# Optimization experiments

Measured on AMD Instinct MI355X. Metric: run time of the kernel, lower is better.

## Reference

```python
import jax, jax.numpy as jnp
import numpy as np

B = 32           # graphs in batch
N_PER = 512      # nodes per graph
N = B * N_PER    # 16384 total nodes (block-diagonal batched graph)
E = N * 16       # 262144 edges
D_IN = 128
D_OUT = 128
ASSIGN = 2048    # total clusters = B * K
K = ASSIGN // B  # 64 clusters per graph


def setup_inputs() -> dict:
    key = jax.random.key(0)
    ks = jax.random.split(key, 6)
    h = jax.random.normal(ks[0], (N, D_IN), jnp.float32)
    # edges confined within each graph -> block-diagonal batched adjacency
    gid = jnp.repeat(jnp.arange(B), E // B)
    edge_src = (jax.random.randint(ks[1], (E,), 0, N_PER) + gid * N_PER).astype(jnp.int32)
    edge_dst = (jax.random.randint(ks[2], (E,), 0, N_PER) + gid * N_PER).astype(jnp.int32)
    # GraphSage NodeApply linears: Linear(2*in, out)
    stdv_f = 1.0 / np.sqrt(2 * D_IN)
    W_feat = jax.random.uniform(ks[3], (2 * D_IN, D_OUT), jnp.float32, -stdv_f, stdv_f)
    b_feat = jnp.zeros((D_OUT,), jnp.float32)
    W_pool = jax.random.uniform(ks[4], (2 * D_IN, ASSIGN), jnp.float32, -stdv_f, stdv_f)
    b_pool = jnp.zeros((ASSIGN,), jnp.float32)
    return {"h": h, "W_feat": W_feat, "b_feat": b_feat,
            "W_pool": W_pool, "b_pool": b_pool,
            "edge_src": edge_src, "edge_dst": edge_dst}


def _graphsage(h, W, b, src, dst):
    # mean aggregation over in-neighbors (dropout=0, batch_norm off)
    msg = jax.ops.segment_sum(h[src], dst, num_segments=N)          # [N, d_in]
    deg = jax.ops.segment_sum(jnp.ones((src.shape[0],), h.dtype), dst, num_segments=N)
    h_neigh = msg / jnp.maximum(deg, 1.0)[:, None]
    bundle = jnp.concatenate([h, h_neigh], axis=1) @ W + b          # [N, d_out]
    # F.normalize(p=2, dim=1) then activation, as in GraphSage NodeApply
    norm = jnp.linalg.norm(bundle, axis=1, keepdims=True)
    bundle = bundle / jnp.maximum(norm, 1e-12)
    return jax.nn.relu(bundle)


def _forward(h, W_feat, b_feat, W_pool, b_pool, src, dst):
    feat = _graphsage(h, W_feat, b_feat, src, dst)       # [N, D_OUT]
    assign = _graphsage(h, W_pool, b_pool, src, dst)     # [N, ASSIGN]
    # block-diagonal mask: node i of graph g may only assign to g's K clusters
    gid_n = jnp.arange(N) // N_PER                       # [N]
    gid_c = jnp.arange(ASSIGN) // K                      # [ASSIGN]
    mask = (gid_n[:, None] == gid_c[None, :]).astype(jnp.float32)
    # masked_softmax with memory_efficient=False
    s = jax.nn.softmax(assign * mask, axis=-1) * mask
    s = s / (s.sum(axis=-1, keepdims=True) + 1e-13)      # [N, ASSIGN]
    h_new = s.T @ feat                                   # [ASSIGN, D_OUT]
    # adj_new = S^T A S without densifying A: (A S)[dst] += S[src]
    a_s = jax.ops.segment_sum(s[src], dst, num_segments=N)
    adj_new = s.T @ a_s                                  # [ASSIGN, ASSIGN]
    return adj_new, h_new


def reference(h, W_feat, b_feat, W_pool, b_pool, edge_src, edge_dst):
    return _forward(h, W_feat, b_feat, W_pool, b_pool, edge_src, edge_dst)
```

## Files before the change

### kernel.cpp

```cpp
#include <hip/hip_runtime.h>

#define NB   32
#define NPER 512
#define NN   16384
#define EE   262144
#define DD   128
#define AS   2048
#define KC   64

using short8   = __attribute__((ext_vector_type(8))) short;
using floatx4  = __attribute__((ext_vector_type(4))) float;
using ushort4v = __attribute__((ext_vector_type(4))) unsigned short;

typedef __attribute__((address_space(3))) unsigned int lds_u32;
typedef const __attribute__((address_space(1))) unsigned int gbl_u32;

static __device__ __forceinline__ void gload16(const unsigned short* g, unsigned short* l) {
    __builtin_amdgcn_global_load_lds((gbl_u32*)g, (lds_u32*)l, 16, 0, 0);
}

static __device__ __forceinline__ float bits2f(unsigned int u) {
    union { unsigned int i; float f; } z; z.i = u << 16; return z.f;
}
static __device__ __forceinline__ unsigned short f2b(float x) {
    union { float f; unsigned int u; } v; v.f = x;
    unsigned int r = v.u + 0x7fffu + ((v.u >> 16) & 1u);
    return (unsigned short)(r >> 16);
}

__global__ void prep_kernel(const float* __restrict__ h, unsigned short* __restrict__ bundle,
                            unsigned short* __restrict__ hT, const int* __restrict__ esrc,
                            const int* __restrict__ edst, unsigned int* __restrict__ Acnt) {
    __shared__ unsigned short fT[128 * 136];
    int b = blockIdx.x, t = threadIdx.x;
    if (b < 128) {
        int node0 = b * 128;
        int r = t >> 1, hf = t & 1;
        const float4* h4 = reinterpret_cast<const float4*>(h + (size_t)(node0 + r) * 128 + hf * 64);
        unsigned short* bo = bundle + (size_t)(node0 + r) * 256 + hf * 64;
#pragma unroll
        for (int i = 0; i < 16; i++) {
            float4 v = h4[i];
            ushort4v o = { f2b(v.x), f2b(v.y), f2b(v.z), f2b(v.w) };
            *reinterpret_cast<ushort4v*>(bo + 4 * i) = o;
            int c = hf * 64 + 4 * i;
            fT[(c + 0) * 136 + r] = o.x;
            fT[(c + 1) * 136 + r] = o.y;
            fT[(c + 2) * 136 + r] = o.z;
            fT[(c + 3) * 136 + r] = o.w;
        }
        __syncthreads();
        int c = t >> 1, nh = t & 1;
        const uint4* src = reinterpret_cast<const uint4*>(&fT[c * 136 + nh * 64]);
        uint4* dst = reinterpret_cast<uint4*>(hT + (size_t)c * NN + node0 + nh * 64);
#pragma unroll
        for (int i = 0; i < 8; i++) dst[i] = src[i];
    } else {
        int e = (b - 128) * 256 + t;
        int d = edst[e], sl = esrc[e] & 511;
        int idx = d * 512 + sl;
        atomicAdd(&Acnt[idx >> 2], 1u << (8 * (idx & 3)));
    }
}

__global__ void conv_kernel(const unsigned int* __restrict__ Acnt,
                            unsigned short* __restrict__ Aadj, float* __restrict__ invdeg) {
    int t = threadIdx.x;
    int row = blockIdx.x * 8 + (t >> 5);
    int u = t & 31;
    uint4 w = reinterpret_cast<const uint4*>(Acnt)[(size_t)row * 32 + u];
    unsigned int wa[4] = { w.x, w.y, w.z, w.w };
    unsigned short out[16];
    float sum = 0.f;
#pragma unroll
    for (int i = 0; i < 4; i++) {
#pragma unroll
        for (int bb = 0; bb < 4; bb++) {
            float fv = (float)((wa[i] >> (8 * bb)) & 0xffu);
            sum += fv;
            out[4 * i + bb] = f2b(fv);
        }
    }
    unsigned int pw[8];
#pragma unroll
    for (int i = 0; i < 8; i++)
        pw[i] = (unsigned int)out[2 * i] | ((unsigned int)out[2 * i + 1] << 16);
    uint4* dst = reinterpret_cast<uint4*>(Aadj + (size_t)row * 512 + u * 16);
    uint4 s0 = { pw[0], pw[1], pw[2], pw[3] }, s1 = { pw[4], pw[5], pw[6], pw[7] };
    dst[0] = s0; dst[1] = s1;
#pragma unroll
    for (int d = 1; d < 32; d <<= 1) sum += __shfl_xor(sum, d, 64);
    if (u == 0) invdeg[row] = 1.0f / fmaxf(sum, 1.0f);
}

__global__ void transpose_cast2_kernel(const float* __restrict__ Wf, const float* __restrict__ Wp,
                                       unsigned short* __restrict__ WfT, unsigned short* __restrict__ WpT) {
    __shared__ float tl[32][33];
    int tx = threadIdx.x, ty = threadIdx.y;
    int bx = blockIdx.x;
    const float* in; unsigned short* out; int C, cb;
    if (bx < DD / 32) { in = Wf; out = WfT; C = DD; cb = bx; }
    else              { in = Wp; out = WpT; C = AS; cb = bx - DD / 32; }
    int c0 = cb * 32, r0 = blockIdx.y * 32;
    for (int i = 0; i < 4; i++)
        tl[ty + 8 * i][tx] = in[(size_t)(r0 + ty + 8 * i) * C + c0 + tx];
    __syncthreads();
    for (int i = 0; i < 4; i++)
        out[(size_t)(c0 + ty + 8 * i) * 256 + r0 + tx] = f2b(tl[tx][ty + 8 * i]);
}

__global__ __launch_bounds__(256) void agg_h_mfma_kernel(
    const unsigned short* __restrict__ Aadj, const unsigned short* __restrict__ hT,
    const float* __restrict__ invdeg, unsigned short* __restrict__ bundle) {
    __shared__ alignas(16) unsigned short lA[64 * 512];
    int tid = threadIdx.x, bx = blockIdx.x;
    int r0 = bx * 64, g = bx >> 3;
    int wv = tid >> 6, lane = tid & 63, q = lane >> 4, lm = lane & 15;
    int mw = wv >> 1, nw = wv & 1;
#pragma unroll
    for (int j = 0; j < 16; j++) {
        int u = tid + 256 * j;
        int row = u >> 6, cu = (u & 63) ^ (row & 7);
        gload16(Aadj + (size_t)(r0 + row) * 512 + cu * 8, &lA[u * 8]);
    }
    floatx4 acc[2][4];
#pragma unroll
    for (int mt = 0; mt < 2; mt++)
#pragma unroll
        for (int nt = 0; nt < 4; nt++) acc[mt][nt] = (floatx4)0.f;
    __syncthreads();

    const unsigned short* Bb = hT + (size_t)(64 * nw + lm) * NN + g * 512 + (q << 3);
    short8 bF[2][4];
#pragma unroll
    for (int nt = 0; nt < 4; nt++)
        bF[0][nt] = *reinterpret_cast<const short8*>(Bb + (size_t)16 * nt * NN);
    for (int ki = 0; ki < 16; ki++) {
        if (ki < 15) {
#pragma unroll
            for (int nt = 0; nt < 4; nt++)
                bF[(ki + 1) & 1][nt] =
                    *reinterpret_cast<const short8*>(Bb + (size_t)16 * nt * NN + (ki + 1) * 32);
        }
        short8 aF[2];
        int swz = (4 * ki + q) ^ (lm & 7);
#pragma unroll
        for (int mt = 0; mt < 2; mt++)
            aF[mt] = *reinterpret_cast<const short8*>(&lA[((32 * mw + 16 * mt + lm) * 64 + swz) * 8]);
#pragma unroll
        for (int mt = 0; mt < 2; mt++)
#pragma unroll
            for (int nt = 0; nt < 4; nt++)
                acc[mt][nt] = __builtin_amdgcn_mfma_f32_16x16x32_bf16(aF[mt], bF[ki & 1][nt],
                                                                      acc[mt][nt], 0, 0, 0);
    }
#pragma unroll
    for (int mt = 0; mt < 2; mt++)
#pragma unroll
        for (int r = 0; r < 4; r++) {
            int row = 32 * mw + 16 * mt + 4 * q + r;
            float inv = invdeg[r0 + row];
#pragma unroll
            for (int nt = 0; nt < 4; nt++)
                bundle[(size_t)(r0 + row) * 256 + 128 + 64 * nw + 16 * nt + lm] =
                    f2b(acc[mt][nt][r] * inv);
        }
}

__global__ __launch_bounds__(256) void feat_mfma_kernel(
    const unsigned short* __restrict__ bundle, const unsigned short* __restrict__ WfT,
    const float* __restrict__ bfe, unsigned short* __restrict__ featT) {
    __shared__ alignas(16) unsigned short lA[512 * 8];
    __shared__ alignas(16) unsigned short lB[512 * 8];
    __shared__ float red[256];
    __shared__ alignas(16) unsigned short fT[128 * 136];
    int tid = threadIdx.x;
    int r0 = blockIdx.x * 128;
    int wv = tid >> 6, lane = tid & 63;
    int mw = wv >> 1, nw = wv & 1, q = lane >> 4, lm = lane & 15;
    int rowS0 = tid >> 2,         cS0 = (tid & 3) ^ ((rowS0 >> 1) & 3);
    int rowS1 = (tid + 256) >> 2, cS1 = ((tid + 256) & 3) ^ ((rowS1 >> 1) & 3);
    int swz = q ^ ((lm >> 1) & 3);

    floatx4 acc[4][4];
#pragma unroll
    for (int mi = 0; mi < 4; mi++)
#pragma unroll
        for (int ni = 0; ni < 4; ni++) acc[mi][ni] = (floatx4)0.f;

    for (int k0 = 0; k0 < 256; k0 += 32) {
        gload16(bundle + (size_t)(r0 + rowS0) * 256 + k0 + 8 * cS0, &lA[tid * 8]);
        gload16(bundle + (size_t)(r0 + rowS1) * 256 + k0 + 8 * cS1, &lA[(tid + 256) * 8]);
        gload16(WfT + (size_t)rowS0 * 256 + k0 + 8 * cS0, &lB[tid * 8]);
        gload16(WfT + (size_t)rowS1 * 256 + k0 + 8 * cS1, &lB[(tid + 256) * 8]);
        __syncthreads();
        short8 aF[4], bF[4];
#pragma unroll
        for (int mi = 0; mi < 4; mi++)
            aF[mi] = *reinterpret_cast<const short8*>(&lA[((64 * mw + 16 * mi + lm) * 4 + swz) * 8]);
#pragma unroll
        for (int ni = 0; ni < 4; ni++)
            bF[ni] = *reinterpret_cast<const short8*>(&lB[((64 * nw + 16 * ni + lm) * 4 + swz) * 8]);
#pragma unroll
        for (int mi = 0; mi < 4; mi++)
#pragma unroll
            for (int ni = 0; ni < 4; ni++)
                acc[mi][ni] = __builtin_amdgcn_mfma_f32_16x16x32_bf16(aF[mi], bF[ni], acc[mi][ni], 0, 0, 0);
        __syncthreads();
    }
#pragma unroll
    for (int ni = 0; ni < 4; ni++) {
        float bv = bfe[64 * nw + 16 * ni + lm];
#pragma unroll
        for (int mi = 0; mi < 4; mi++)
#pragma unroll
            for (int r = 0; r < 4; r++) acc[mi][ni][r] += bv;
    }
#pragma unroll
    for (int mi = 0; mi < 4; mi++)
#pragma unroll
        for (int r = 0; r < 4; r++) {
            float p = 0.f;
#pragma unroll
            for (int ni = 0; ni < 4; ni++) p += acc[mi][ni][r] * acc[mi][ni][r];
            p += __shfl_xor(p, 1, 64);
            p += __shfl_xor(p, 2, 64);
            p += __shfl_xor(p, 4, 64);
            p += __shfl_xor(p, 8, 64);
            if (lm == 0) red[nw * 128 + 64 * mw + 16 * mi + 4 * q + r] = p;
        }
    __syncthreads();
#pragma unroll
    for (int mi = 0; mi < 4; mi++) {
        float rrn[4];
#pragma unroll
        for (int r = 0; r < 4; r++) {
            int rl = 64 * mw + 16 * mi + 4 * q + r;
            rrn[r] = 1.0f / fmaxf(sqrtf(red[rl] + red[128 + rl]), 1e-12f);
        }
#pragma unroll
        for (int ni = 0; ni < 4; ni++) {
            int col = 64 * nw + 16 * ni + lm;
            ushort4v pk = { f2b(fmaxf(acc[mi][ni][0] * rrn[0], 0.f)),
                            f2b(fmaxf(acc[mi][ni][1] * rrn[1], 0.f)),
                            f2b(fmaxf(acc[mi][ni][2] * rrn[2], 0.f)),
                            f2b(fmaxf(acc[mi][ni][3] * rrn[3], 0.f)) };
            *reinterpret_cast<ushort4v*>(&fT[col * 136 + 64 * mw + 16 * mi + 4 * q]) = pk;
        }
    }
    __syncthreads();
    {
        int col = tid >> 1, half = tid & 1;
        const uint4* src = reinterpret_cast<const uint4*>(&fT[col * 136 + half * 64]);
        uint4* dst = reinterpret_cast<uint4*>(featT + (size_t)col * NN + r0 + half * 64);
#pragma unroll
        for (int i = 0; i < 8; i++) dst[i] = src[i];
    }
}

__global__ __launch_bounds__(256) void pool_fused_kernel(
    const unsigned short* __restrict__ bundle, const unsigned short* __restrict__ WpT,
    const float* __restrict__ bp, unsigned short* __restrict__ sT) {
    __shared__ alignas(16) unsigned short lA[2048 * 8];
    __shared__ float raw[64 * 68];
    __shared__ float ssq_l[4 * 64];
    __shared__ float rn_l[64];
    int tid = threadIdx.x, bx = blockIdx.x;
    int r0 = bx * 64, g = bx >> 3;
    int wv = tid >> 6, lane = tid & 63, q = lane >> 4, lm = lane & 15;

#pragma unroll
    for (int j = 0; j < 8; j++) {
        int u = tid + 256 * j;
        int row = u >> 5;
        int chunk = (u & 31) ^ (row & 7);
        gload16(bundle + (size_t)(r0 + row) * 256 + chunk * 8, &lA[u * 8]);
    }
    float ssqacc[4][4];
#pragma unroll
    for (int mi = 0; mi < 4; mi++)
#pragma unroll
        for (int r = 0; r < 4; r++) ssqacc[mi][r] = 0.f;
    __syncthreads();

    for (int nc8 = 0; nc8 < 8; nc8++) {
        int nc = 4 * nc8 + wv;
        const unsigned short* Bb = WpT + ((size_t)(nc * 64 + lm) << 8) + (q << 3);
        short8 bF[2][4];
#pragma unroll
        for (int ni = 0; ni < 4; ni++)
            bF[0][ni] = *reinterpret_cast<const short8*>(Bb + (ni << 12));
        floatx4 acc[4][4];
#pragma unroll
        for (int mi = 0; mi < 4; mi++)
#pragma unroll
            for (int ni = 0; ni < 4; ni++) acc[mi][ni] = (floatx4)0.f;
#pragma unroll
        for (int k = 0; k < 8; k++) {
            if (k < 7) {
#pragma unroll
                for (int ni = 0; ni < 4; ni++)
                    bF[(k + 1) & 1][ni] =
                        *reinterpret_cast<const short8*>(Bb + (ni << 12) + ((k + 1) << 5));
            }
            short8 aF[4];
            int swz = (4 * k + q) ^ (lm & 7);
#pragma unroll
            for (int mi = 0; mi < 4; mi++)
                aF[mi] = *reinterpret_cast<const short8*>(&lA[((16 * mi + lm) * 32 + swz) * 8]);
#pragma unroll
            for (int mi = 0; mi < 4; mi++)
#pragma unroll
                for (int ni = 0; ni < 4; ni++)
                    acc[mi][ni] = __builtin_amdgcn_mfma_f32_16x16x32_bf16(aF[mi], bF[k & 1][ni],
                                                                          acc[mi][ni], 0, 0, 0);
        }
        float bv[4];
#pragma unroll
        for (int ni = 0; ni < 4; ni++) bv[ni] = bp[nc * 64 + 16 * ni + lm];
#pragma unroll
        for (int mi = 0; mi < 4; mi++)
#pragma unroll
            for (int r = 0; r < 4; r++) {
                float p = 0.f;
#pragma unroll
                for (int ni = 0; ni < 4; ni++) {
                    acc[mi][ni][r] += bv[ni];
                    p += acc[mi][ni][r] * acc[mi][ni][r];
                }
                ssqacc[mi][r] += p;
            }
        if (nc == g) {
#pragma unroll
            for (int mi = 0; mi < 4; mi++)
#pragma unroll
                for (int ni = 0; ni < 4; ni++)
#pragma unroll
                    for (int r = 0; r < 4; r++)
                        raw[(16 * mi + 4 * q + r) * 68 + 16 * ni + lm] = acc[mi][ni][r];
        }
    }
#pragma unroll
    for (int mi = 0; mi < 4; mi++)
#pragma unroll
        for (int r = 0; r < 4; r++) {
            float p = ssqacc[mi][r];
            p += __shfl_xor(p, 1, 64);
            p += __shfl_xor(p, 2, 64);
            p += __shfl_xor(p, 4, 64);
            p += __shfl_xor(p, 8, 64);
            if (lm == 0) ssq_l[wv * 64 + 16 * mi + 4 * q + r] = p;
        }
    __syncthreads();
    if (tid < 64)
        rn_l[tid] = 1.0f / fmaxf(sqrtf(ssq_l[tid] + ssq_l[64 + tid] + ssq_l[128 + tid] +
                                       ssq_l[192 + tid]), 1e-12f);
    __syncthreads();
    {
        int row = tid >> 2, j = tid & 3;
        int nloc = ((bx & 7) << 6) + row;
        float rn = rn_l[row];
        float v[16];
        float mx = -1e30f;
#pragma unroll
        for (int c4 = 0; c4 < 4; c4++) {
            float4 rv = *reinterpret_cast<const float4*>(&raw[row * 68 + 16 * j + 4 * c4]);
            v[4 * c4 + 0] = fmaxf(rv.x * rn, 0.f);
            v[4 * c4 + 1] = fmaxf(rv.y * rn, 0.f);
            v[4 * c4 + 2] = fmaxf(rv.z * rn, 0.f);
            v[4 * c4 + 3] = fmaxf(rv.w * rn, 0.f);
        }
#pragma unroll
        for (int c = 0; c < 16; c++) mx = fmaxf(mx, v[c]);
        mx = fmaxf(mx, __shfl_xor(mx, 1, 64));
        mx = fmaxf(mx, __shfl_xor(mx, 2, 64));
        float z = 0.f;
#pragma unroll
        for (int c = 0; c < 16; c++) { v[c] = __expf(v[c] - mx); z += v[c]; }
        z += __shfl_xor(z, 1, 64);
        z += __shfl_xor(z, 2, 64);
        float iz = 1.0f / z;
#pragma unroll
        for (int c4 = 0; c4 < 4; c4++) {
            size_t tb = (size_t)(g * KC + 16 * j + 4 * c4) * NPER + nloc;
            sT[tb] = f2b(v[4 * c4 + 0] * iz);
            sT[tb + NPER] = f2b(v[4 * c4 + 1] * iz);
            sT[tb + 2 * NPER] = f2b(v[4 * c4 + 2] * iz);
            sT[tb + 3 * NPER] = f2b(v[4 * c4 + 3] * iz);
        }
    }
}

__global__ __launch_bounds__(256) void as_mfma_kernel(
    const unsigned short* __restrict__ sT, const unsigned short* __restrict__ Aadj,
    unsigned short* __restrict__ asT) {
    __shared__ alignas(16) unsigned short lS[64 * 512];
    int tid = threadIdx.x, bx = blockIdx.x;
    int g = bx >> 1, half = bx & 1;
    int wv = tid >> 6, lane = tid & 63, q = lane >> 4, lm = lane & 15;
#pragma unroll
    for (int j = 0; j < 16; j++) {
        int u = tid + 256 * j;
        int row = u >> 6, cu = (u & 63) ^ (row & 7);
        gload16(sT + (size_t)(g * KC + row) * NPER + cu * 8, &lS[u * 8]);
    }
    floatx4 acc[4][4];
#pragma unroll
    for (int mi = 0; mi < 4; mi++)
#pragma unroll
        for (int nt = 0; nt < 4; nt++) acc[mi][nt] = (floatx4)0.f;
    __syncthreads();

    int dbase = half * 256 + wv * 64;
    const unsigned short* Bb = Aadj + (size_t)(g * 512 + dbase + lm) * 512 + (q << 3);
    short8 bF[2][4];
#pragma unroll
    for (int nt = 0; nt < 4; nt++)
        bF[0][nt] = *reinterpret_cast<const short8*>(Bb + (size_t)16 * nt * 512);
    for (int ki = 0; ki < 16; ki++) {
        if (ki < 15) {
#pragma unroll
            for (int nt = 0; nt < 4; nt++)
                bF[(ki + 1) & 1][nt] =
                    *reinterpret_cast<const short8*>(Bb + (size_t)16 * nt * 512 + (ki + 1) * 32);
        }
        short8 aF[4];
        int swz = (4 * ki + q) ^ (lm & 7);
#pragma unroll
        for (int mi = 0; mi < 4; mi++)
            aF[mi] = *reinterpret_cast<const short8*>(&lS[((16 * mi + lm) * 64 + swz) * 8]);
#pragma unroll
        for (int mi = 0; mi < 4; mi++)
#pragma unroll
            for (int nt = 0; nt < 4; nt++)
                acc[mi][nt] = __builtin_amdgcn_mfma_f32_16x16x32_bf16(aF[mi], bF[ki & 1][nt],
                                                                      acc[mi][nt], 0, 0, 0);
    }
#pragma unroll
    for (int mi = 0; mi < 4; mi++)
#pragma unroll
        for (int r = 0; r < 4; r++) {
            int row = 16 * mi + 4 * q + r;
#pragma unroll
            for (int nt = 0; nt < 4; nt++)
                asT[(size_t)(g * KC + row) * NPER + dbase + 16 * nt + lm] = f2b(acc[mi][nt][r]);
        }
}

__global__ __launch_bounds__(256) void hnew_adj_kernel(
    const unsigned short* __restrict__ sT, const unsigned short* __restrict__ featT,
    const unsigned short* __restrict__ asT, float* __restrict__ adjf,
    float* __restrict__ hnewf) {
    __shared__ alignas(16) unsigned short lS[1024 * 8];
    __shared__ alignas(16) unsigned short lF[2048 * 8];
    __shared__ alignas(16) unsigned short lAS[1024 * 8];
    int tid = threadIdx.x;
    int ch = blockIdx.x, g = blockIdx.y;
    int k0 = g * NPER + ch * 128;
    int wv = tid >> 6, lane = tid & 63, q = lane >> 4, lm = lane & 15;

#pragma unroll
    for (int j = 0; j < 4; j++) {
        int u = tid + 256 * j;
        int row = u >> 4, cu = (u & 15) ^ (row & 15);
        gload16(sT + (size_t)(g * KC + row) * NPER + ch * 128 + cu * 8, &lS[u * 8]);
    }
#pragma unroll
    for (int j = 0; j < 8; j++) {
        int u = tid + 256 * j;
        int row = u >> 4, cu = (u & 15) ^ (row & 15);
        gload16(featT + (size_t)row * NN + k0 + cu * 8, &lF[u * 8]);
    }
#pragma unroll
    for (int j = 0; j < 4; j++) {
        int u = tid + 256 * j;
        int row = u >> 4, cu = (u & 15) ^ (row & 15);
        gload16(asT + (size_t)(g * KC + row) * NPER + ch * 128 + cu * 8, &lAS[u * 8]);
    }
    floatx4 acc[4][4];
#pragma unroll
    for (int mi = 0; mi < 4; mi++)
#pragma unroll
        for (int ni = 0; ni < 4; ni++) acc[mi][ni] = (floatx4)0.f;
    __syncthreads();

    bool isH = (wv < 2);
    for (int ks = 0; ks < 4; ks++) {
        if (!isH && (ks >> 1) != (wv & 1)) continue;
        short8 aF[4], bF[4];
#pragma unroll
        for (int mi = 0; mi < 4; mi++)
            aF[mi] = *reinterpret_cast<const short8*>(
                &lS[((16 * mi + lm) * 16 + ((4 * ks + q) ^ lm)) * 8]);
        if (isH) {
#pragma unroll
            for (int ni = 0; ni < 4; ni++)
                bF[ni] = *reinterpret_cast<const short8*>(
                    &lF[((64 * wv + 16 * ni + lm) * 16 + ((4 * ks + q) ^ lm)) * 8]);
        } else {
#pragma unroll
            for (int ni = 0; ni < 4; ni++)
                bF[ni] = *reinterpret_cast<const short8*>(
                    &lAS[((16 * ni + lm) * 16 + ((4 * ks + q) ^ lm)) * 8]);
        }
#pragma unroll
        for (int mi = 0; mi < 4; mi++)
#pragma unroll
            for (int ni = 0; ni < 4; ni++)
                acc[mi][ni] = __builtin_amdgcn_mfma_f32_16x16x32_bf16(aF[mi], bF[ni], acc[mi][ni], 0, 0, 0);
    }
    if (isH) {
#pragma unroll
        for (int mi = 0; mi < 4; mi++)
#pragma unroll
            for (int ni = 0; ni < 4; ni++)
#pragma unroll
                for (int r = 0; r < 4; r++)
                    atomicAdd(&hnewf[(size_t)(g * KC + 16 * mi + 4 * q + r) * DD +
                                     64 * wv + 16 * ni + lm], acc[mi][ni][r]);
    } else {
#pragma unroll
        for (int mi = 0; mi < 4; mi++)
#pragma unroll
            for (int ni = 0; ni < 4; ni++)
#pragma unroll
                for (int r = 0; r < 4; r++)
                    atomicAdd(&adjf[(size_t)(g * KC + 16 * mi + 4 * q + r) * AS +
                                    g * KC + 16 * ni + lm], acc[mi][ni][r]);
    }
}

extern "C" void kernel_launch(void* const* d_in, const int* in_sizes, int n_in,
                              void* d_out, int out_size, void* d_ws, size_t ws_size,
                              hipStream_t stream) {
    const float* h   = (const float*)d_in[0];
    const float* Wf  = (const float*)d_in[1];
    const float* bfe = (const float*)d_in[2];
    const float* Wp  = (const float*)d_in[3];
    const float* bp  = (const float*)d_in[4];
    const int* esrc  = (const int*)d_in[5];
    const int* edst  = (const int*)d_in[6];

    float* adjf  = (float*)d_out;
    float* hnewf = adjf + (size_t)AS * AS;

    unsigned short* bundle = (unsigned short*)d_ws;
    unsigned short* WfT   = bundle + (size_t)NN * 256;
    unsigned short* WpT   = WfT + 128 * 256;
    unsigned short* sT    = WpT + (size_t)AS * 256;
    unsigned short* asT   = sT + (size_t)NN * KC;
    unsigned short* featT = asT + (size_t)NN * KC;
    unsigned short* hT    = featT + (size_t)DD * NN;
    unsigned short* Aadj  = hT + (size_t)DD * NN;
    float* invdeg = (float*)(Aadj + (size_t)NN * 512);
    unsigned int* Acnt = (unsigned int*)(invdeg + NN);

    hipMemsetAsync(Acnt, 0, (size_t)NN * 512, stream);
    hipMemsetAsync(d_out, 0, ((size_t)AS * AS + (size_t)AS * DD) * sizeof(float), stream);

    prep_kernel<<<128 + EE / 256, 256, 0, stream>>>(h, bundle, hT, esrc, edst, Acnt);
    conv_kernel<<<NN / 8, 256, 0, stream>>>(Acnt, Aadj, invdeg);
    transpose_cast2_kernel<<<dim3(DD / 32 + AS / 32, 256 / 32), dim3(32, 8), 0, stream>>>(
        Wf, Wp, WfT, WpT);
    agg_h_mfma_kernel<<<NN / 64, 256, 0, stream>>>(Aadj, hT, invdeg, bundle);
    feat_mfma_kernel<<<NN / 128, 256, 0, stream>>>(bundle, WfT, bfe, featT);
    pool_fused_kernel<<<NN / 64, 256, 0, stream>>>(bundle, WpT, bp, sT);
    as_mfma_kernel<<<NB * 2, 256, 0, stream>>>(sT, Aadj, asT);
    hnew_adj_kernel<<<dim3(4, NB), 256, 0, stream>>>(sT, featT, asT, adjf, hnewf);
}
```

Baseline: 185.7 us.

## Fuse all stages into one cooperative persistent kernel with grid syncs

Replaces the two memsets and eight separate kernel launches with a single cooperative mega-kernel of 256 persistent blocks. Each stage runs as a grid-strided tile loop, stages are separated by grid.sync(), and a union sizes shared memory for the largest stage. This removes per-launch overhead and inter-kernel gaps. The cost is one-block-per-CU occupancy (launch_bounds 256,1, with LDS sized to the largest stage), stages with fewer tiles than blocks leaving CUs idle, and grid barrier cost. The old multi-kernel path stays as a fallback if the cooperative launch fails.

Measured after the change: 519.1 us. 180% more time.

```diff
diff --git a/kernel.cpp b/kernel.cpp
--- a/kernel.cpp
+++ b/kernel.cpp
@@ -1,4 +1,7 @@
 #include <hip/hip_runtime.h>
+#include <hip/hip_cooperative_groups.h>
+
+namespace cg = cooperative_groups;
 
 #define NB   32
 #define NPER 512
@@ -7,6 +10,7 @@
 #define DD   128
 #define AS   2048
 #define KC   64
+#define GRID 256
 
 using short8   = __attribute__((ext_vector_type(8))) short;
 using floatx4  = __attribute__((ext_vector_type(4))) float;
@@ -27,6 +31,518 @@
     unsigned int r = v.u + 0x7fffu + ((v.u >> 16) & 1u);
     return (unsigned short)(r >> 16);
 }
+
+union __align__(16) SMem {
+    unsigned short big[32768];
+    struct { unsigned short lA[16384]; float raw[4352]; float ssq[256]; float rn[64]; } pool;
+    struct { unsigned short lA[4096]; unsigned short lB[4096]; float red[256];
+             unsigned short fT[17408]; } feat;
+    struct { unsigned short lS[8192]; unsigned short lF[16384]; unsigned short lAS[8192]; } ha;
+    struct { unsigned short fT[17408]; } prep;
+    struct { float tl[32][33]; } tr;
+};
+
+__global__ __launch_bounds__(256, 1) void mega_kernel(
+    const float* __restrict__ h, const float* __restrict__ Wf, const float* __restrict__ bfe,
+    const float* __restrict__ Wp, const float* __restrict__ bp,
+    const int* __restrict__ esrc, const int* __restrict__ edst,
+    float* __restrict__ adjf, float* __restrict__ hnewf,
+    unsigned short* __restrict__ bundle, unsigned short* __restrict__ WfT,
+    unsigned short* __restrict__ WpT, unsigned short* __restrict__ sT,
+    unsigned short* __restrict__ asT, unsigned short* __restrict__ featT,
+    unsigned short* __restrict__ hT, unsigned short* __restrict__ Aadj,
+    float* __restrict__ invdeg, unsigned int* __restrict__ Acnt) {
+    __shared__ SMem sm;
+    cg::grid_group grid = cg::this_grid();
+    int tid = threadIdx.x;
+    int gtid = blockIdx.x * 256 + tid;
+
+    {
+        uint4 z = {0u, 0u, 0u, 0u};
+        uint4* A4 = reinterpret_cast<uint4*>(Acnt);
+        for (int i = gtid; i < 524288; i += GRID * 256) A4[i] = z;
+        uint4* O4 = reinterpret_cast<uint4*>(adjf);
+        for (int i = gtid; i < 1114112; i += GRID * 256) O4[i] = z;
+    }
+    __threadfence();
+    grid.sync();
+
+    for (int t = blockIdx.x; t < 1696; t += GRID) {
+        if (t < 128) {
+            int node0 = t * 128;
+            int r = tid >> 1, hf = tid & 1;
+            const float4* h4 = reinterpret_cast<const float4*>(h + (size_t)(node0 + r) * 128 + hf * 64);
+            unsigned short* bo = bundle + (size_t)(node0 + r) * 256 + hf * 64;
+#pragma unroll
+            for (int i = 0; i < 16; i++) {
+                float4 v = h4[i];
+                ushort4v o = { f2b(v.x), f2b(v.y), f2b(v.z), f2b(v.w) };
+                *reinterpret_cast<ushort4v*>(bo + 4 * i) = o;
+                int c = hf * 64 + 4 * i;
+                sm.prep.fT[(c + 0) * 136 + r] = o.x;
+                sm.prep.fT[(c + 1) * 136 + r] = o.y;
+                sm.prep.fT[(c + 2) * 136 + r] = o.z;
+                sm.prep.fT[(c + 3) * 136 + r] = o.w;
+            }
+            __syncthreads();
+            int c = tid >> 1, nh = tid & 1;
+            const uint4* src = reinterpret_cast<const uint4*>(&sm.prep.fT[c * 136 + nh * 64]);
+            uint4* dst = reinterpret_cast<uint4*>(hT + (size_t)c * NN + node0 + nh * 64);
+#pragma unroll
+            for (int i = 0; i < 8; i++) dst[i] = src[i];
+        } else if (t < 1152) {
+            int e = (t - 128) * 256 + tid;
+            int d = edst[e], sl = esrc[e] & 511;
+            int idx = d * 512 + sl;
+            atomicAdd(&Acnt[idx >> 2], 1u << (8 * (idx & 3)));
+        } else {
+            int tb = t - 1152;
+            int bx = tb % 68, by = tb / 68;
+            int tx = tid & 31, ty = tid >> 5;
+            const float* in; unsigned short* out; int C, cb;
+            if (bx < DD / 32) { in = Wf; out = WfT; C = DD; cb = bx; }
+            else              { in = Wp; out = WpT; C = AS; cb = bx - DD / 32; }
+            int c0 = cb * 32, r0 = by * 32;
+            for (int i = 0; i < 4; i++)
+                sm.tr.tl[ty + 8 * i][tx] = in[(size_t)(r0 + ty + 8 * i) * C + c0 + tx];
+            __syncthreads();
+            for (int i = 0; i < 4; i++)
+                out[(size_t)(c0 + ty + 8 * i) * 256 + r0 + tx] = f2b(sm.tr.tl[tx][ty + 8 * i]);
+        }
+        __syncthreads();
+    }
+    __threadfence();
+    grid.sync();
+
+    for (int t = blockIdx.x; t < 2048; t += GRID) {
+        int row = t * 8 + (tid >> 5);
+        int u = tid & 31;
+        uint4 w = reinterpret_cast<const uint4*>(Acnt)[(size_t)row * 32 + u];
+        unsigned int wa[4] = { w.x, w.y, w.z, w.w };
+        unsigned short out[16];
+        float sum = 0.f;
+#pragma unroll
+        for (int i = 0; i < 4; i++) {
+#pragma unroll
+            for (int bb = 0; bb < 4; bb++) {
+                float fv = (float)((wa[i] >> (8 * bb)) & 0xffu);
+                sum += fv;
+                out[4 * i + bb] = f2b(fv);
+            }
+        }
+        unsigned int pw[8];
+#pragma unroll
+        for (int i = 0; i < 8; i++)
+            pw[i] = (unsigned int)out[2 * i] | ((unsigned int)out[2 * i + 1] << 16);
+        uint4* dst = reinterpret_cast<uint4*>(Aadj + (size_t)row * 512 + u * 16);
+        uint4 s0 = { pw[0], pw[1], pw[2], pw[3] }, s1 = { pw[4], pw[5], pw[6], pw[7] };
+        dst[0] = s0; dst[1] = s1;
+#pragma unroll
+        for (int d = 1; d < 32; d <<= 1) sum += __shfl_xor(sum, d, 64);
+        if (u == 0) invdeg[row] = 1.0f / fmaxf(sum, 1.0f);
+    }
+    __threadfence();
+    grid.sync();
+
+    for (int bx = blockIdx.x; bx < 256; bx += GRID) {
+        int r0 = bx * 64, g = bx >> 3;
+        int wv = tid >> 6, lane = tid & 63, q = lane >> 4, lm = lane & 15;
+        int mw = wv >> 1, nw = wv & 1;
+#pragma unroll
+        for (int j = 0; j < 16; j++) {
+            int u = tid + 256 * j;
+            int row = u >> 6, cu = (u & 63) ^ (row & 7);
+            gload16(Aadj + (size_t)(r0 + row) * 512 + cu * 8, &sm.big[u * 8]);
+        }
+        floatx4 acc[2][4];
+#pragma unroll
+        for (int mt = 0; mt < 2; mt++)
+#pragma unroll
+            for (int nt = 0; nt < 4; nt++) acc[mt][nt] = (floatx4)0.f;
+        __syncthreads();
+
+        const unsigned short* Bb = hT + (size_t)(64 * nw + lm) * NN + g * 512 + (q << 3);
+        short8 bF[2][4];
+#pragma unroll
+        for (int nt = 0; nt < 4; nt++)
+            bF[0][nt] = *reinterpret_cast<const short8*>(Bb + (size_t)16 * nt * NN);
+        for (int ki = 0; ki < 16; ki++) {
+            if (ki < 15) {
+#pragma unroll
+                for (int nt = 0; nt < 4; nt++)
+                    bF[(ki + 1) & 1][nt] =
+                        *reinterpret_cast<const short8*>(Bb + (size_t)16 * nt * NN + (ki + 1) * 32);
+            }
+            short8 aF[2];
+            int swz = (4 * ki + q) ^ (lm & 7);
+#pragma unroll
+            for (int mt = 0; mt < 2; mt++)
+                aF[mt] = *reinterpret_cast<const short8*>(&sm.big[((32 * mw + 16 * mt + lm) * 64 + swz) * 8]);
+#pragma unroll
+            for (int mt = 0; mt < 2; mt++)
+#pragma unroll
+                for (int nt = 0; nt < 4; nt++)
+                    acc[mt][nt] = __builtin_amdgcn_mfma_f32_16x16x32_bf16(aF[mt], bF[ki & 1][nt],
+                                                                          acc[mt][nt], 0, 0, 0);
+        }
+#pragma unroll
+        for (int mt = 0; mt < 2; mt++)
+#pragma unroll
+            for (int r = 0; r < 4; r++) {
+                int row = 32 * mw + 16 * mt + 4 * q + r;
+                float inv = invdeg[r0 + row];
+#pragma unroll
+                for (int nt = 0; nt < 4; nt++)
+                    bundle[(size_t)(r0 + row) * 256 + 128 + 64 * nw + 16 * nt + lm] =
+                        f2b(acc[mt][nt][r] * inv);
+            }
+        __syncthreads();
+    }
+    __threadfence();
+    grid.sync();
+
+    for (int t = blockIdx.x; t < 384; t += GRID) {
+        if (t < 128) {
+            int r0 = t * 128;
+            int wv = tid >> 6, lane = tid & 63;
+            int mw = wv >> 1, nw = wv & 1, q = lane >> 4, lm = lane & 15;
+            int rowS0 = tid >> 2,         cS0 = (tid & 3) ^ ((rowS0 >> 1) & 3);
+            int rowS1 = (tid + 256) >> 2, cS1 = ((tid + 256) & 3) ^ ((rowS1 >> 1) & 3);
+            int swz = q ^ ((lm >> 1) & 3);
+            floatx4 acc[4][4];
+#pragma unroll
+            for (int mi = 0; mi < 4; mi++)
+#pragma unroll
+                for (int ni = 0; ni < 4; ni++) acc[mi][ni] = (floatx4)0.f;
+            for (int k0 = 0; k0 < 256; k0 += 32) {
+                gload16(bundle + (size_t)(r0 + rowS0) * 256 + k0 + 8 * cS0, &sm.feat.lA[tid * 8]);
+                gload16(bundle + (size_t)(r0 + rowS1) * 256 + k0 + 8 * cS1, &sm.feat.lA[(tid + 256) * 8]);
+                gload16(WfT + (size_t)rowS0 * 256 + k0 + 8 * cS0, &sm.feat.lB[tid * 8]);
+                gload16(WfT + (size_t)rowS1 * 256 + k0 + 8 * cS1, &sm.feat.lB[(tid + 256) * 8]);
+                __syncthreads();
+                short8 aF[4], bF[4];
+#pragma unroll
+                for (int mi = 0; mi < 4; mi++)
+                    aF[mi] = *reinterpret_cast<const short8*>(&sm.feat.lA[((64 * mw + 16 * mi + lm) * 4 + swz) * 8]);
+#pragma unroll
+                for (int ni = 0; ni < 4; ni++)
+                    bF[ni] = *reinterpret_cast<const short8*>(&sm.feat.lB[((64 * nw + 16 * ni + lm) * 4 + swz) * 8]);
+#pragma unroll
+                for (int mi = 0; mi < 4; mi++)
+#pragma unroll
+                    for (int ni = 0; ni < 4; ni++)
+                        acc[mi][ni] = __builtin_amdgcn_mfma_f32_16x16x32_bf16(aF[mi], bF[ni], acc[mi][ni], 0, 0, 0);
+                __syncthreads();
+            }
+#pragma unroll
+            for (int ni = 0; ni < 4; ni++) {
+                float bv = bfe[64 * nw + 16 * ni + lm];
+#pragma unroll
+                for (int mi = 0; mi < 4; mi++)
+#pragma unroll
+                    for (int r = 0; r < 4; r++) acc[mi][ni][r] += bv;
+            }
+#pragma unroll
+            for (int mi = 0; mi < 4; mi++)
+#pragma unroll
+                for (int r = 0; r < 4; r++) {
+                    float p = 0.f;
+#pragma unroll
+                    for (int ni = 0; ni < 4; ni++) p += acc[mi][ni][r] * acc[mi][ni][r];
+                    p += __shfl_xor(p, 1, 64);
+                    p += __shfl_xor(p, 2, 64);
+                    p += __shfl_xor(p, 4, 64);
+                    p += __shfl_xor(p, 8, 64);
+                    if (lm == 0) sm.feat.red[nw * 128 + 64 * mw + 16 * mi + 4 * q + r] = p;
+                }
+            __syncthreads();
+#pragma unroll
+            for (int mi = 0; mi < 4; mi++) {
+                float rrn[4];
+#pragma unroll
+                for (int r = 0; r < 4; r++) {
+                    int rl = 64 * mw + 16 * mi + 4 * q + r;
+                    rrn[r] = 1.0f / fmaxf(sqrtf(sm.feat.red[rl] + sm.feat.red[128 + rl]), 1e-12f);
+                }
+#pragma unroll
+                for (int ni = 0; ni < 4; ni++) {
+                    int col = 64 * nw + 16 * ni + lm;
+                    ushort4v pk = { f2b(fmaxf(acc[mi][ni][0] * rrn[0], 0.f)),
+                                    f2b(fmaxf(acc[mi][ni][1] * rrn[1], 0.f)),
+                                    f2b(fmaxf(acc[mi][ni][2] * rrn[2], 0.f)),
+                                    f2b(fmaxf(acc[mi][ni][3] * rrn[3], 0.f)) };
+                    *reinterpret_cast<ushort4v*>(&sm.feat.fT[col * 136 + 64 * mw + 16 * mi + 4 * q]) = pk;
+                }
+            }
+            __syncthreads();
+            {
+                int col = tid >> 1, half = tid & 1;
+                const uint4* src = reinterpret_cast<const uint4*>(&sm.feat.fT[col * 136 + half * 64]);
+                uint4* dst = reinterpret_cast<uint4*>(featT + (size_t)col * NN + r0 + half * 64);
+#pragma unroll
+                for (int i = 0; i < 8; i++) dst[i] = src[i];
+            }
+        } else {
+            int bx = t - 128;
+            int r0 = bx * 64, g = bx >> 3;
+            int wv = tid >> 6, lane = tid & 63, q = lane >> 4, lm = lane & 15;
+#pragma unroll
+            for (int j = 0; j < 8; j++) {
+                int u = tid + 256 * j;
+                int row = u >> 5;
+                int chunk = (u & 31) ^ (row & 7);
+                gload16(bundle + (size_t)(r0 + row) * 256 + chunk * 8, &sm.pool.lA[u * 8]);
+            }
+            float ssqacc[4][4];
+#pragma unroll
+            for (int mi = 0; mi < 4; mi++)
+#pragma unroll
+                for (int r = 0; r < 4; r++) ssqacc[mi][r] = 0.f;
+            __syncthreads();
+            for (int nc8 = 0; nc8 < 8; nc8++) {
+                int nc = 4 * nc8 + wv;
+                const unsigned short* Bb = WpT + ((size_t)(nc * 64 + lm) << 8) + (q << 3);
+                short8 bF[2][4];
+#pragma unroll
+                for (int ni = 0; ni < 4; ni++)
+                    bF[0][ni] = *reinterpret_cast<const short8*>(Bb + (ni << 12));
+                floatx4 acc[4][4];
+#pragma unroll
+                for (int mi = 0; mi < 4; mi++)
+#pragma unroll
+                    for (int ni = 0; ni < 4; ni++) acc[mi][ni] = (floatx4)0.f;
+#pragma unroll
+                for (int k = 0; k < 8; k++) {
+                    if (k < 7) {
+#pragma unroll
+                        for (int ni = 0; ni < 4; ni++)
+                            bF[(k + 1) & 1][ni] =
+                                *reinterpret_cast<const short8*>(Bb + (ni << 12) + ((k + 1) << 5));
+                    }
+                    short8 aF[4];
+                    int swz = (4 * k + q) ^ (lm & 7);
+#pragma unroll
+                    for (int mi = 0; mi < 4; mi++)
+                        aF[mi] = *reinterpret_cast<const short8*>(&sm.pool.lA[((16 * mi + lm) * 32 + swz) * 8]);
+#pragma unroll
+                    for (int mi = 0; mi < 4; mi++)
+#pragma unroll
+                        for (int ni = 0; ni < 4; ni++)
+                            acc[mi][ni] = __builtin_amdgcn_mfma_f32_16x16x32_bf16(aF[mi], bF[k & 1][ni],
+                                                                                  acc[mi][ni], 0, 0, 0);
+                }
+                float bv[4];
+#pragma unroll
+                for (int ni = 0; ni < 4; ni++) bv[ni] = bp[nc * 64 + 16 * ni + lm];
+#pragma unroll
+                for (int mi = 0; mi < 4; mi++)
+#pragma unroll
+                    for (int r = 0; r < 4; r++) {
+                        float p = 0.f;
+#pragma unroll
+                        for (int ni = 0; ni < 4; ni++) {
+                            acc[mi][ni][r] += bv[ni];
+                            p += acc[mi][ni][r] * acc[mi][ni][r];
+                        }
+                        ssqacc[mi][r] += p;
+                    }
+                if (nc == g) {
+#pragma unroll
+                    for (int mi = 0; mi < 4; mi++)
+#pragma unroll
+                        for (int ni = 0; ni < 4; ni++)
+#pragma unroll
+                            for (int r = 0; r < 4; r++)
+                                sm.pool.raw[(16 * mi + 4 * q + r) * 68 + 16 * ni + lm] = acc[mi][ni][r];
+                }
+            }
+#pragma unroll
+            for (int mi = 0; mi < 4; mi++)
+#pragma unroll
+                for (int r = 0; r < 4; r++) {
+                    float p = ssqacc[mi][r];
+                    p += __shfl_xor(p, 1, 64);
+                    p += __shfl_xor(p, 2, 64);
+                    p += __shfl_xor(p, 4, 64);
+                    p += __shfl_xor(p, 8, 64);
+                    if (lm == 0) sm.pool.ssq[wv * 64 + 16 * mi + 4 * q + r] = p;
+                }
+            __syncthreads();
+            if (tid < 64)
+                sm.pool.rn[tid] = 1.0f / fmaxf(sqrtf(sm.pool.ssq[tid] + sm.pool.ssq[64 + tid] +
+                                               sm.pool.ssq[128 + tid] + sm.pool.ssq[192 + tid]), 1e-12f);
+            __syncthreads();
+            {
+                int row = tid >> 2, j = tid & 3;
+                int nloc = ((bx & 7) << 6) + row;
+                float rn = sm.pool.rn[row];
+                float v[16];
+                float mx = -1e30f;
+#pragma unroll
+                for (int c4 = 0; c4 < 4; c4++) {
+                    float4 rv = *reinterpret_cast<const float4*>(&sm.pool.raw[row * 68 + 16 * j + 4 * c4]);
+                    v[4 * c4 + 0] = fmaxf(rv.x * rn, 0.f);
+                    v[4 * c4 + 1] = fmaxf(rv.y * rn, 0.f);
+                    v[4 * c4 + 2] = fmaxf(rv.z * rn, 0.f);
+                    v[4 * c4 + 3] = fmaxf(rv.w * rn, 0.f);
+                }
+#pragma unroll
+                for (int c = 0; c < 16; c++) mx = fmaxf(mx, v[c]);
+                mx = fmaxf(mx, __shfl_xor(mx, 1, 64));
+                mx = fmaxf(mx, __shfl_xor(mx, 2, 64));
+                float z = 0.f;
+#pragma unroll
+                for (int c = 0; c < 16; c++) { v[c] = __expf(v[c] - mx); z += v[c]; }
+                z += __shfl_xor(z, 1, 64);
+                z += __shfl_xor(z, 2, 64);
+                float iz = 1.0f / z;
+#pragma unroll
+                for (int c4 = 0; c4 < 4; c4++) {
+                    size_t tb = (size_t)(g * KC + 16 * j + 4 * c4) * NPER + nloc;
+                    sT[tb] = f2b(v[4 * c4 + 0] * iz);
+                    sT[tb + NPER] = f2b(v[4 * c4 + 1] * iz);
+                    sT[tb + 2 * NPER] = f2b(v[4 * c4 + 2] * iz);
+                    sT[tb + 3 * NPER] = f2b(v[4 * c4 + 3] * iz);
+                }
+            }
+        }
+        __syncthreads();
+    }
+    __threadfence();
+    grid.sync();
+
+    for (int bx = blockIdx.x; bx < NB * 2; bx += GRID) {
+        int g = bx >> 1, half = bx & 1;
+        int wv = tid >> 6, lane = tid & 63, q = lane >> 4, lm = lane & 15;
+#pragma unroll
+        for (int j = 0; j < 16; j++) {
+            int u = tid + 256 * j;
+            int row = u >> 6, cu = (u & 63) ^ (row & 7);
+            gload16(sT + (size_t)(g * KC + row) * NPER + cu * 8, &sm.big[u * 8]);
+        }
+        floatx4 acc[4][4];
+#pragma unroll
+        for (int mi = 0; mi < 4; mi++)
+#pragma unroll
+            for (int nt = 0; nt < 4; nt++) acc[mi][nt] = (floatx4)0.f;
+        __syncthreads();
+
+        int dbase = half * 256 + wv * 64;
+        const unsigned short* Bb = Aadj + (size_t)(g * 512 + dbase + lm) * 512 + (q << 3);
+        short8 bF[2][4];
+#pragma unroll
+        for (int nt = 0; nt < 4; nt++)
+            bF[0][nt] = *reinterpret_cast<const short8*>(Bb + (size_t)16 * nt * 512);
+        for (int ki = 0; ki < 16; ki++) {
+            if (ki < 15) {
+#pragma unroll
+                for (int nt = 0; nt < 4; nt++)
+                    bF[(ki + 1) & 1][nt] =
+                        *reinterpret_cast<const short8*>(Bb + (size_t)16 * nt * 512 + (ki + 1) * 32);
+            }
+            short8 aF[4];
+            int swz = (4 * ki + q) ^ (lm & 7);
+#pragma unroll
+            for (int mi = 0; mi < 4; mi++)
+                aF[mi] = *reinterpret_cast<const short8*>(&sm.big[((16 * mi + lm) * 64 + swz) * 8]);
+#pragma unroll
+            for (int mi = 0; mi < 4; mi++)
+#pragma unroll
+                for (int nt = 0; nt < 4; nt++)
+                    acc[mi][nt] = __builtin_amdgcn_mfma_f32_16x16x32_bf16(aF[mi], bF[ki & 1][nt],
+                                                                          acc[mi][nt], 0, 0, 0);
+        }
+#pragma unroll
+        for (int mi = 0; mi < 4; mi++)
+#pragma unroll
+            for (int r = 0; r < 4; r++) {
+                int row = 16 * mi + 4 * q + r;
+#pragma unroll
+                for (int nt = 0; nt < 4; nt++)
+                    asT[(size_t)(g * KC + row) * NPER + dbase + 16 * nt + lm] = f2b(acc[mi][nt][r]);
+            }
+        __syncthreads();
+    }
+    __threadfence();
+    grid.sync();
+
+    for (int t = blockIdx.x; t < 128; t += GRID) {
+        int ch = t & 3, g = t >> 2;
+        int k0 = g * NPER + ch * 128;
+        int wv = tid >> 6, lane = tid & 63, q = lane >> 4, lm = lane & 15;
+#pragma unroll
+        for (int j = 0; j < 4; j++) {
+            int u = tid + 256 * j;
+            int row = u >> 4, cu = (u & 15) ^ (row & 15);
+            gload16(sT + (size_t)(g * KC + row) * NPER + ch * 128 + cu * 8, &sm.ha.lS[u * 8]);
+        }
+#pragma unroll
+        for (int j = 0; j < 8; j++) {
+            int u = tid + 256 * j;
+            int row = u >> 4, cu = (u & 15) ^ (row & 15);
+            gload16(featT + (size_t)row * NN + k0 + cu * 8, &sm.ha.lF[u * 8]);
+        }
+#pragma unroll
+        for (int j = 0; j < 4; j++) {
+            int u = tid + 256 * j;
+            int row = u >> 4, cu = (u & 15) ^ (row & 15);
+            gload16(asT + (size_t)(g * KC + row) * NPER + ch * 128 + cu * 8, &sm.ha.lAS[u * 8]);
+        }
+        floatx4 acc[4][4];
+#pragma unroll
+        for (int mi = 0; mi < 4; mi++)
+#pragma unroll
+            for (int ni = 0; ni < 4; ni++) acc[mi][ni] = (floatx4)0.f;
+        __syncthreads();
+
+        bool isH = (wv < 2);
+        for (int ks = 0; ks < 4; ks++) {
+            if (!isH && (ks >> 1) != (wv & 1)) continue;
+            short8 aF[4], bF[4];
+#pragma unroll
+            for (int mi = 0; mi < 4; mi++)
+                aF[mi] = *reinterpret_cast<const short8*>(
+                    &sm.ha.lS[((16 * mi + lm) * 16 + ((4 * ks + q) ^ lm)) * 8]);
+            if (isH) {
+#pragma unroll
+                for (int ni = 0; ni < 4; ni++)
+                    bF[ni] = *reinterpret_cast<const short8*>(
+                        &sm.ha.lF[((64 * wv + 16 * ni + lm) * 16 + ((4 * ks + q) ^ lm)) * 8]);
+            } else {
+#pragma unroll
+                for (int ni = 0; ni < 4; ni++)
+                    bF[ni] = *reinterpret_cast<const short8*>(
+                        &sm.ha.lAS[((16 * ni + lm) * 16 + ((4 * ks + q) ^ lm)) * 8]);
+            }
+#pragma unroll
+            for (int mi = 0; mi < 4; mi++)
+#pragma unroll
+                for (int ni = 0; ni < 4; ni++)
+                    acc[mi][ni] = __builtin_amdgcn_mfma_f32_16x16x32_bf16(aF[mi], bF[ni], acc[mi][ni], 0, 0, 0);
+        }
+        if (isH) {
+#pragma unroll
+            for (int mi = 0; mi < 4; mi++)
+#pragma unroll
+                for (int ni = 0; ni < 4; ni++)
+#pragma unroll
+                    for (int r = 0; r < 4; r++)
+                        atomicAdd(&hnewf[(size_t)(g * KC + 16 * mi + 4 * q + r) * DD +
+                                         64 * wv + 16 * ni + lm], acc[mi][ni][r]);
+        } else {
+#pragma unroll
+            for (int mi = 0; mi < 4; mi++)
+#pragma unroll
+                for (int ni = 0; ni < 4; ni++)
+#pragma unroll
+                    for (int r = 0; r < 4; r++)
+                        atomicAdd(&adjf[(size_t)(g * KC + 16 * mi + 4 * q + r) * AS +
+                                        g * KC + 16 * ni + lm], acc[mi][ni][r]);
+        }
+        __syncthreads();
+    }
+}
+
 
 __global__ void prep_kernel(const float* __restrict__ h, unsigned short* __restrict__ bundle,
                             unsigned short* __restrict__ hT, const int* __restrict__ esrc,
@@ -129,7 +645,6 @@
 #pragma unroll
         for (int nt = 0; nt < 4; nt++) acc[mt][nt] = (floatx4)0.f;
     __syncthreads();
-
     const unsigned short* Bb = hT + (size_t)(64 * nw + lm) * NN + g * 512 + (q << 3);
     short8 bF[2][4];
 #pragma unroll
@@ -181,13 +696,11 @@
     int rowS0 = tid >> 2,         cS0 = (tid & 3) ^ ((rowS0 >> 1) & 3);
     int rowS1 = (tid + 256) >> 2, cS1 = ((tid + 256) & 3) ^ ((rowS1 >> 1) & 3);
     int swz = q ^ ((lm >> 1) & 3);
-
     floatx4 acc[4][4];
 #pragma unroll
     for (int mi = 0; mi < 4; mi++)
 #pragma unroll
         for (int ni = 0; ni < 4; ni++) acc[mi][ni] = (floatx4)0.f;
-
     for (int k0 = 0; k0 < 256; k0 += 32) {
         gload16(bundle + (size_t)(r0 + rowS0) * 256 + k0 + 8 * cS0, &lA[tid * 8]);
         gload16(bundle + (size_t)(r0 + rowS1) * 256 + k0 + 8 * cS1, &lA[(tid + 256) * 8]);
@@ -268,7 +781,6 @@
     int tid = threadIdx.x, bx = blockIdx.x;
     int r0 = bx * 64, g = bx >> 3;
     int wv = tid >> 6, lane = tid & 63, q = lane >> 4, lm = lane & 15;
-
 #pragma unroll
     for (int j = 0; j < 8; j++) {
         int u = tid + 256 * j;
@@ -282,7 +794,6 @@
 #pragma unroll
         for (int r = 0; r < 4; r++) ssqacc[mi][r] = 0.f;
     __syncthreads();
-
     for (int nc8 = 0; nc8 < 8; nc8++) {
         int nc = 4 * nc8 + wv;
         const unsigned short* Bb = WpT + ((size_t)(nc * 64 + lm) << 8) + (q << 3);
@@ -410,7 +921,6 @@
 #pragma unroll
         for (int nt = 0; nt < 4; nt++) acc[mi][nt] = (floatx4)0.f;
     __syncthreads();
-
     int dbase = half * 256 + wv * 64;
     const unsigned short* Bb = Aadj + (size_t)(g * 512 + dbase + lm) * 512 + (q << 3);
     short8 bF[2][4];
@@ -458,7 +968,6 @@
     int ch = blockIdx.x, g = blockIdx.y;
     int k0 = g * NPER + ch * 128;
     int wv = tid >> 6, lane = tid & 63, q = lane >> 4, lm = lane & 15;
-
 #pragma unroll
     for (int j = 0; j < 4; j++) {
         int u = tid + 256 * j;
@@ -483,7 +992,6 @@
 #pragma unroll
         for (int ni = 0; ni < 4; ni++) acc[mi][ni] = (floatx4)0.f;
     __syncthreads();
-
     bool isH = (wv < 2);
     for (int ks = 0; ks < 4; ks++) {
         if (!isH && (ks >> 1) != (wv & 1)) continue;
@@ -555,16 +1063,23 @@
     float* invdeg = (float*)(Aadj + (size_t)NN * 512);
     unsigned int* Acnt = (unsigned int*)(invdeg + NN);
 
-    hipMemsetAsync(Acnt, 0, (size_t)NN * 512, stream);
-    hipMemsetAsync(d_out, 0, ((size_t)AS * AS + (size_t)AS * DD) * sizeof(float), stream);
-
-    prep_kernel<<<128 + EE / 256, 256, 0, stream>>>(h, bundle, hT, esrc, edst, Acnt);
-    conv_kernel<<<NN / 8, 256, 0, stream>>>(Acnt, Aadj, invdeg);
-    transpose_cast2_kernel<<<dim3(DD / 32 + AS / 32, 256 / 32), dim3(32, 8), 0, stream>>>(
-        Wf, Wp, WfT, WpT);
-    agg_h_mfma_kernel<<<NN / 64, 256, 0, stream>>>(Aadj, hT, invdeg, bundle);
-    feat_mfma_kernel<<<NN / 128, 256, 0, stream>>>(bundle, WfT, bfe, featT);
-    pool_fused_kernel<<<NN / 64, 256, 0, stream>>>(bundle, WpT, bp, sT);
-    as_mfma_kernel<<<NB * 2, 256, 0, stream>>>(sT, Aadj, asT);
-    hnew_adj_kernel<<<dim3(4, NB), 256, 0, stream>>>(sT, featT, asT, adjf, hnewf);
-}
+    void* kargs[] = { (void*)&h, (void*)&Wf, (void*)&bfe, (void*)&Wp, (void*)&bp,
+                      (void*)&esrc, (void*)&edst, (void*)&adjf, (void*)&hnewf,
+                      (void*)&bundle, (void*)&WfT, (void*)&WpT, (void*)&sT, (void*)&asT,
+                      (void*)&featT, (void*)&hT, (void*)&Aadj, (void*)&invdeg, (void*)&Acnt };
+    hipError_t err = hipLaunchCooperativeKernel((void*)mega_kernel, dim3(GRID), dim3(256),
+                                                kargs, 0, stream);
+    if (err != hipSuccess) {
+        hipMemsetAsync(Acnt, 0, (size_t)NN * 512, stream);
+        hipMemsetAsync(d_out, 0, ((size_t)AS * AS + (size_t)AS * DD) * sizeof(float), stream);
+        prep_kernel<<<128 + EE / 256, 256, 0, stream>>>(h, bundle, hT, esrc, edst, Acnt);
+        conv_kernel<<<NN / 8, 256, 0, stream>>>(Acnt, Aadj, invdeg);
+        transpose_cast2_kernel<<<dim3(DD / 32 + AS / 32, 256 / 32), dim3(32, 8), 0, stream>>>(
+            Wf, Wp, WfT, WpT);
+        agg_h_mfma_kernel<<<NN / 64, 256, 0, stream>>>(Aadj, hT, invdeg, bundle);
+        feat_mfma_kernel<<<NN / 128, 256, 0, stream>>>(bundle, WfT, bfe, featT);
+        pool_fused_kernel<<<NN / 64, 256, 0, stream>>>(bundle, WpT, bp, sT);
+        as_mfma_kernel<<<NB * 2, 256, 0, stream>>>(sT, Aadj, asT);
+        hnew_adj_kernel<<<dim3(4, NB), 256, 0, stream>>>(sT, featT, asT, adjf, hnewf);
+    }
+}
```
